# Kernel optimization log

Hardware: AMD Instinct MI355X
Metric: run time of the kernel (lower is better)

The kernel has to match this reference:

```python
import jax, jax.numpy as jnp
import numpy as np

N_NODES = 100000  # graph size (set via set_features/adj_lists in the original)
DEGREE = 32       # sampled neighbors per node (num_sample)
N_PAIRS = 8192    # link-prediction batch
FEAT_DIM = 9      # nn.Embedding(18, 9)
HID = 20          # enc1 embed_dim
OUT = 15          # n_out / enc2 embed_dim


def setup_inputs() -> dict:
    key = jax.random.key(0)
    ks = jax.random.split(key, 9)
    to_pred = jax.random.randint(ks[0], (N_PAIRS, 2), 0, N_NODES)
    adj = jax.random.randint(ks[1], (N_NODES, DEGREE), 0, N_NODES)
    feat = jax.random.normal(ks[2], (N_NODES, FEAT_DIM), dtype=jnp.float32)
    W1 = jax.random.normal(ks[3], (HID, 2 * FEAT_DIM), dtype=jnp.float32) * 0.1
    W2 = jax.random.normal(ks[4], (OUT, HID), dtype=jnp.float32) * 0.1
    fc1_w = jax.random.normal(ks[5], (15, 30), dtype=jnp.float32) * 0.1
    fc1_b = jnp.zeros((15,), dtype=jnp.float32)
    fc2_w = jax.random.normal(ks[6], (1, 15), dtype=jnp.float32) * 0.1
    fc2_b = jnp.zeros((1,), dtype=jnp.float32)
    return {"to_pred": to_pred, "adj": adj, "feat": feat, "W1": W1, "W2": W2,
            "fc1_w": fc1_w, "fc1_b": fc1_b, "fc2_w": fc2_w, "fc2_b": fc2_b}


def _enc1(nodes, feat, adj, W1):
    # GraphSAGE layer 1 (gcn=False): concat(self, mean(neighbors)) -> relu(W1 @ .)
    neigh_feat = feat[adj[nodes]].mean(axis=-2)          # [..., FEAT_DIM]
    combined = jnp.concatenate([feat[nodes], neigh_feat], axis=-1)  # [..., 2*FEAT_DIM]
    return jax.nn.relu(combined @ W1.T)                  # [..., HID]


def _enc2(nodes, feat, adj, W1, W2):
    # GraphSAGE layer 2 (gcn=True): neighbor set includes self, mean-only aggregate
    neighs = jnp.concatenate([adj[nodes], nodes[:, None]], axis=-1)  # [B, K+1]
    h1 = _enc1(neighs, feat, adj, W1)                    # [B, K+1, HID]
    return jax.nn.relu(h1.mean(axis=1) @ W2.T)           # [B, OUT]


def reference(to_pred, adj, feat, W1, W2, fc1_w, fc1_b, fc2_w, fc2_b):
    # two_fc_link_prediction: embed both endpoints, concat, 2-layer ReLU MLP
    e1 = _enc2(to_pred[:, 0], feat, adj, W1, W2)         # [B, OUT]
    e2 = _enc2(to_pred[:, 1], feat, adj, W1, W2)         # [B, OUT]
    cat = jnp.concatenate([e1, e2], axis=1)              # [B, 30]
    h = jax.nn.relu(cat @ fc1_w.T + fc1_b)               # [B, 15]
    out = jax.nn.relu(h @ fc2_w.T + fc2_b)               # [B, 1]
    return jnp.squeeze(out, axis=-1)                     # [B]
```

## Files before the change

kernel.cpp:

```cpp
#include <hip/hip_runtime.h>
#include <hip/hip_bf16.h>

#define N_NODES 100000
#define DEGREE 32
#define N_PAIRS 8192
#define FEAT 9
#define HID 20
#define NOUT 15

__global__ __launch_bounds__(256) void k_neigh_mean(
    const int* __restrict__ adj,
    const float* __restrict__ feat,
    float* __restrict__ s_ws) {
  int t = blockIdx.x * blockDim.x + threadIdx.x;
  if (t >= N_NODES * FEAT) return;
  int node = t / FEAT;
  int j = t - node * FEAT;
  const int* arow = adj + node * DEGREE;
  float s = 0.f;
#pragma unroll
  for (int k = 0; k < DEGREE; ++k) {
    int m = arow[k];
    s += feat[m * FEAT + j];
  }
  s_ws[t] = s * (1.0f / DEGREE);
}

__global__ __launch_bounds__(256) void k_node_embed(
    const float* __restrict__ feat,
    const float* __restrict__ s_ws,
    const float* __restrict__ W1,
    const float* __restrict__ W2,
    float* __restrict__ t_ws) {
  __shared__ float sW1[HID * 2 * FEAT];
  __shared__ float sW2[NOUT * HID];
  for (int i = threadIdx.x; i < HID * 2 * FEAT; i += blockDim.x)
    sW1[i] = W1[i];
  for (int i = threadIdx.x; i < NOUT * HID; i += blockDim.x)
    sW2[i] = W2[i];
  __syncthreads();

  int n = blockIdx.x * blockDim.x + threadIdx.x;
  if (n >= N_NODES) return;

  float comb[2 * FEAT];
#pragma unroll
  for (int j = 0; j < FEAT; ++j) comb[j] = feat[n * FEAT + j];
#pragma unroll
  for (int j = 0; j < FEAT; ++j) comb[FEAT + j] = s_ws[n * FEAT + j];

  float h1[HID];
#pragma unroll
  for (int i = 0; i < HID; ++i) {
    float acc = 0.f;
#pragma unroll
    for (int j = 0; j < 2 * FEAT; ++j) acc += sW1[i * 2 * FEAT + j] * comb[j];
    h1[i] = fmaxf(acc, 0.f);
  }
#pragma unroll
  for (int d = 0; d < NOUT; ++d) {
    float acc = 0.f;
#pragma unroll
    for (int i = 0; i < HID; ++i) acc += sW2[d * HID + i] * h1[i];
    t_ws[n * NOUT + d] = acc;
  }
}

__global__ __launch_bounds__(256) void k_endpoint(
    const int* __restrict__ to_pred,
    const int* __restrict__ adj,
    const float* __restrict__ t_ws,
    float* __restrict__ e_ws) {
  int t = blockIdx.x * blockDim.x + threadIdx.x;
  if (t >= 2 * N_PAIRS * NOUT) return;
  int ep = t / NOUT;
  int d = t - ep * NOUT;
  int node = to_pred[ep];
  const int* arow = adj + node * DEGREE;
  float s = t_ws[node * NOUT + d];
#pragma unroll
  for (int k = 0; k < DEGREE; ++k) {
    int m = arow[k];
    s += t_ws[m * NOUT + d];
  }
  e_ws[t] = fmaxf(s * (1.0f / (DEGREE + 1)), 0.f);
}

__global__ __launch_bounds__(256) void k_mlp(
    const float* __restrict__ e_ws,
    const float* __restrict__ fc1_w,
    const float* __restrict__ fc1_b,
    const float* __restrict__ fc2_w,
    const float* __restrict__ fc2_b,
    float* __restrict__ out) {
  __shared__ float s1[15 * 30];
  __shared__ float b1[15];
  __shared__ float s2[15];
  __shared__ float b2;
  for (int i = threadIdx.x; i < 15 * 30; i += blockDim.x)
    s1[i] = fc1_w[i];
  if (threadIdx.x < 15) {
    b1[threadIdx.x] = fc1_b[threadIdx.x];
    s2[threadIdx.x] = fc2_w[threadIdx.x];
  }
  if (threadIdx.x == 0) b2 = fc2_b[0];
  __syncthreads();

  int p = blockIdx.x * blockDim.x + threadIdx.x;
  if (p >= N_PAIRS) return;

  float cat[30];
#pragma unroll
  for (int j = 0; j < 30; ++j) cat[j] = e_ws[p * 30 + j];

  float acc2 = b2;
#pragma unroll
  for (int i = 0; i < 15; ++i) {
    float acc = b1[i];
#pragma unroll
    for (int j = 0; j < 30; ++j) acc += s1[i * 30 + j] * cat[j];
    acc2 += s2[i] * fmaxf(acc, 0.f);
  }
  out[p] = fmaxf(acc2, 0.f);
}

extern "C" void kernel_launch(void* const* d_in, const int* in_sizes, int n_in,
                              void* d_out, int out_size, void* d_ws,
                              size_t ws_size, hipStream_t stream) {
  const int* to_pred     = (const int*)d_in[0];
  const int* adj         = (const int*)d_in[1];
  const float* feat      = (const float*)d_in[2];
  const float* W1        = (const float*)d_in[3];
  const float* W2        = (const float*)d_in[4];
  const float* fc1_w     = (const float*)d_in[5];
  const float* fc1_b     = (const float*)d_in[6];
  const float* fc2_w     = (const float*)d_in[7];
  const float* fc2_b     = (const float*)d_in[8];
  float* out             = (float*)d_out;

  char* ws = (char*)d_ws;
  float* t_ws = (float*)ws;
  float* s_ws = (float*)(ws + 6000000);
  float* e_ws = (float*)(ws + 9600000);

  {
    int total = N_NODES * FEAT;
    k_neigh_mean<<<(total + 255) / 256, 256, 0, stream>>>(adj, feat, s_ws);
  }
  {
    int total = N_NODES;
    k_node_embed<<<(total + 255) / 256, 256, 0, stream>>>(feat, s_ws, W1, W2,
                                                          t_ws);
  }
  {
    int total = 2 * N_PAIRS * NOUT;
    k_endpoint<<<(total + 255) / 256, 256, 0, stream>>>(to_pred, adj, t_ws,
                                                        e_ws);
  }
  {
    int total = N_PAIRS;
    k_mlp<<<(total + 255) / 256, 256, 0, stream>>>(e_ws, fc1_w, fc1_b, fc2_w,
                                                   fc2_b, out);
  }
}
```

Before: 132.2 us.

## Fuse four kernels into two block-cooperative node and pair kernels

Merges the neighbor-mean gather and the per-node two-layer embedding into one kernel. Each block handles 28 nodes and keeps intermediates in shared memory, so the s_ws round trip and one launch go away. It also fuses the endpoint aggregation with the link MLP, 8 pairs per block, which drops e_ws and another launch. In exchange, thread utilisation is lower: only 252 of 256 threads gather in the first phase and 240 in the pair kernel. Work is also split across several syncthreads phases, and the grid becomes much larger with smaller per-block work.

Result: faster. 119.5 us (-9.6%).

```diff
diff --git a/kernel.cpp b/kernel.cpp
--- a/kernel.cpp
+++ b/kernel.cpp
@@ -8,158 +8,151 @@
 #define HID 20
 #define NOUT 15
 
-__global__ __launch_bounds__(256) void k_neigh_mean(
+#define NPB 28
+#define PPB 8
+
+__global__ __launch_bounds__(256) void k_node_all(
     const int* __restrict__ adj,
     const float* __restrict__ feat,
-    float* __restrict__ s_ws) {
-  int t = blockIdx.x * blockDim.x + threadIdx.x;
-  if (t >= N_NODES * FEAT) return;
-  int node = t / FEAT;
-  int j = t - node * FEAT;
-  const int* arow = adj + node * DEGREE;
-  float s = 0.f;
-#pragma unroll
-  for (int k = 0; k < DEGREE; ++k) {
-    int m = arow[k];
-    s += feat[m * FEAT + j];
-  }
-  s_ws[t] = s * (1.0f / DEGREE);
-}
-
-__global__ __launch_bounds__(256) void k_node_embed(
-    const float* __restrict__ feat,
-    const float* __restrict__ s_ws,
     const float* __restrict__ W1,
     const float* __restrict__ W2,
     float* __restrict__ t_ws) {
   __shared__ float sW1[HID * 2 * FEAT];
   __shared__ float sW2[NOUT * HID];
-  for (int i = threadIdx.x; i < HID * 2 * FEAT; i += blockDim.x)
-    sW1[i] = W1[i];
-  for (int i = threadIdx.x; i < NOUT * HID; i += blockDim.x)
-    sW2[i] = W2[i];
+  __shared__ float sComb[NPB][2 * FEAT];
+  __shared__ float sH[NPB][HID];
+
+  int tid = threadIdx.x;
+  for (int i = tid; i < HID * 2 * FEAT; i += 256) sW1[i] = W1[i];
+  for (int i = tid; i < NOUT * HID; i += 256) sW2[i] = W2[i];
+
+  int base = blockIdx.x * NPB;
+
+  if (tid < NPB * FEAT) {
+    int nl = tid / FEAT;
+    int j = tid - nl * FEAT;
+    int n = base + nl;
+    if (n < N_NODES) {
+      const int* arow = adj + n * DEGREE;
+      float s = 0.f;
+#pragma unroll
+      for (int k = 0; k < DEGREE; ++k) {
+        int m = arow[k];
+        s += feat[m * FEAT + j];
+      }
+      sComb[nl][j] = feat[n * FEAT + j];
+      sComb[nl][FEAT + j] = s * (1.0f / DEGREE);
+    }
+  }
   __syncthreads();
 
-  int n = blockIdx.x * blockDim.x + threadIdx.x;
-  if (n >= N_NODES) return;
+  for (int idx = tid; idx < NPB * HID; idx += 256) {
+    int nl = idx / HID;
+    int i = idx - nl * HID;
+    if (base + nl < N_NODES) {
+      float acc = 0.f;
+#pragma unroll
+      for (int j = 0; j < 2 * FEAT; ++j) acc += sW1[i * 2 * FEAT + j] * sComb[nl][j];
+      sH[nl][i] = fmaxf(acc, 0.f);
+    }
+  }
+  __syncthreads();
 
-  float comb[2 * FEAT];
+  for (int idx = tid; idx < NPB * NOUT; idx += 256) {
+    int nl = idx / NOUT;
+    int d = idx - nl * NOUT;
+    int n = base + nl;
+    if (n < N_NODES) {
+      float acc = 0.f;
 #pragma unroll
-  for (int j = 0; j < FEAT; ++j) comb[j] = feat[n * FEAT + j];
-#pragma unroll
-  for (int j = 0; j < FEAT; ++j) comb[FEAT + j] = s_ws[n * FEAT + j];
-
-  float h1[HID];
-#pragma unroll
-  for (int i = 0; i < HID; ++i) {
-    float acc = 0.f;
-#pragma unroll
-    for (int j = 0; j < 2 * FEAT; ++j) acc += sW1[i * 2 * FEAT + j] * comb[j];
-    h1[i] = fmaxf(acc, 0.f);
-  }
-#pragma unroll
-  for (int d = 0; d < NOUT; ++d) {
-    float acc = 0.f;
-#pragma unroll
-    for (int i = 0; i < HID; ++i) acc += sW2[d * HID + i] * h1[i];
-    t_ws[n * NOUT + d] = acc;
+      for (int i = 0; i < HID; ++i) acc += sW2[d * HID + i] * sH[nl][i];
+      t_ws[n * NOUT + d] = acc;
+    }
   }
 }
 
-__global__ __launch_bounds__(256) void k_endpoint(
+__global__ __launch_bounds__(256) void k_pair_all(
     const int* __restrict__ to_pred,
     const int* __restrict__ adj,
     const float* __restrict__ t_ws,
-    float* __restrict__ e_ws) {
-  int t = blockIdx.x * blockDim.x + threadIdx.x;
-  if (t >= 2 * N_PAIRS * NOUT) return;
-  int ep = t / NOUT;
-  int d = t - ep * NOUT;
-  int node = to_pred[ep];
-  const int* arow = adj + node * DEGREE;
-  float s = t_ws[node * NOUT + d];
-#pragma unroll
-  for (int k = 0; k < DEGREE; ++k) {
-    int m = arow[k];
-    s += t_ws[m * NOUT + d];
-  }
-  e_ws[t] = fmaxf(s * (1.0f / (DEGREE + 1)), 0.f);
-}
-
-__global__ __launch_bounds__(256) void k_mlp(
-    const float* __restrict__ e_ws,
     const float* __restrict__ fc1_w,
     const float* __restrict__ fc1_b,
     const float* __restrict__ fc2_w,
     const float* __restrict__ fc2_b,
     float* __restrict__ out) {
   __shared__ float s1[15 * 30];
-  __shared__ float b1[15];
-  __shared__ float s2[15];
-  __shared__ float b2;
-  for (int i = threadIdx.x; i < 15 * 30; i += blockDim.x)
-    s1[i] = fc1_w[i];
-  if (threadIdx.x < 15) {
-    b1[threadIdx.x] = fc1_b[threadIdx.x];
-    s2[threadIdx.x] = fc2_w[threadIdx.x];
+  __shared__ float b1v[15];
+  __shared__ float s2v[15];
+  __shared__ float b2v;
+  __shared__ float sE[PPB][30];
+  __shared__ float sHh[PPB][15];
+
+  int tid = threadIdx.x;
+  for (int i = tid; i < 15 * 30; i += 256) s1[i] = fc1_w[i];
+  if (tid < 15) {
+    b1v[tid] = fc1_b[tid];
+    s2v[tid] = fc2_w[tid];
   }
-  if (threadIdx.x == 0) b2 = fc2_b[0];
+  if (tid == 0) b2v = fc2_b[0];
+
+  int pbase = blockIdx.x * PPB;
+
+  if (tid < PPB * 30) {
+    int pl = tid / 30;
+    int slot = tid - pl * 30;
+    int side = slot / 15;
+    int d = slot - side * 15;
+    int p = pbase + pl;
+    int node = to_pred[2 * p + side];
+    const int* arow = adj + node * DEGREE;
+    float s = t_ws[node * NOUT + d];
+#pragma unroll
+    for (int k = 0; k < DEGREE; ++k) {
+      int m = arow[k];
+      s += t_ws[m * NOUT + d];
+    }
+    sE[pl][slot] = fmaxf(s * (1.0f / (DEGREE + 1)), 0.f);
+  }
   __syncthreads();
 
-  int p = blockIdx.x * blockDim.x + threadIdx.x;
-  if (p >= N_PAIRS) return;
+  if (tid < PPB * 15) {
+    int pl = tid / 15;
+    int i = tid - pl * 15;
+    float acc = b1v[i];
+#pragma unroll
+    for (int j = 0; j < 30; ++j) acc += s1[i * 30 + j] * sE[pl][j];
+    sHh[pl][i] = fmaxf(acc, 0.f);
+  }
+  __syncthreads();
 
-  float cat[30];
+  if (tid < PPB) {
+    float acc = b2v;
 #pragma unroll
-  for (int j = 0; j < 30; ++j) cat[j] = e_ws[p * 30 + j];
-
-  float acc2 = b2;
-#pragma unroll
-  for (int i = 0; i < 15; ++i) {
-    float acc = b1[i];
-#pragma unroll
-    for (int j = 0; j < 30; ++j) acc += s1[i * 30 + j] * cat[j];
-    acc2 += s2[i] * fmaxf(acc, 0.f);
+    for (int i = 0; i < 15; ++i) acc += s2v[i] * sHh[tid][i];
+    out[pbase + tid] = fmaxf(acc, 0.f);
   }
-  out[p] = fmaxf(acc2, 0.f);
 }
 
 extern "C" void kernel_launch(void* const* d_in, const int* in_sizes, int n_in,
                               void* d_out, int out_size, void* d_ws,
                               size_t ws_size, hipStream_t stream) {
-  const int* to_pred     = (const int*)d_in[0];
-  const int* adj         = (const int*)d_in[1];
-  const float* feat      = (const float*)d_in[2];
-  const float* W1        = (const float*)d_in[3];
-  const float* W2        = (const float*)d_in[4];
-  const float* fc1_w     = (const float*)d_in[5];
-  const float* fc1_b     = (const float*)d_in[6];
-  const float* fc2_w     = (const float*)d_in[7];
-  const float* fc2_b     = (const float*)d_in[8];
-  float* out             = (float*)d_out;
+  const int* to_pred = (const int*)d_in[0];
+  const int* adj     = (const int*)d_in[1];
+  const float* feat  = (const float*)d_in[2];
+  const float* W1    = (const float*)d_in[3];
+  const float* W2    = (const float*)d_in[4];
+  const float* fc1_w = (const float*)d_in[5];
+  const float* fc1_b = (const float*)d_in[6];
+  const float* fc2_w = (const float*)d_in[7];
+  const float* fc2_b = (const float*)d_in[8];
+  float* out         = (float*)d_out;
 
-  char* ws = (char*)d_ws;
-  float* t_ws = (float*)ws;
-  float* s_ws = (float*)(ws + 6000000);
-  float* e_ws = (float*)(ws + 9600000);
+  float* t_ws = (float*)d_ws;
 
-  {
-    int total = N_NODES * FEAT;
-    k_neigh_mean<<<(total + 255) / 256, 256, 0, stream>>>(adj, feat, s_ws);
-  }
-  {
-    int total = N_NODES;
-    k_node_embed<<<(total + 255) / 256, 256, 0, stream>>>(feat, s_ws, W1, W2,
-                                                          t_ws);
-  }
-  {
-    int total = 2 * N_PAIRS * NOUT;
-    k_endpoint<<<(total + 255) / 256, 256, 0, stream>>>(to_pred, adj, t_ws,
-                                                        e_ws);
-  }
-  {
-    int total = N_PAIRS;
-    k_mlp<<<(total + 255) / 256, 256, 0, stream>>>(e_ws, fc1_w, fc1_b, fc2_w,
-                                                   fc2_b, out);
-  }
+  int grid1 = (N_NODES + NPB - 1) / NPB;
+  k_node_all<<<grid1, 256, 0, stream>>>(adj, feat, W1, W2, t_ws);
+
+  int grid2 = N_PAIRS / PPB;
+  k_pair_all<<<grid2, 256, 0, stream>>>(to_pred, adj, t_ws, fc1_w, fc1_b,
+                                        fc2_w, fc2_b, out);
 }
```
